# Kernel tuning notes

Measured on AMD Instinct MI355X. Metric: run time of the kernel, lower is better.

The kernel has to match this reference:

```python
import jax, jax.numpy as jnp
import numpy as np

MUL = 128   # multiplicity of every l in the input/output irreps
C   = 128   # channel count of the grid signal
LIN = 3     # lmax of irreps_in / irreps_out
LV  = 2     # VSH lmax = lmax - 1
NB  = 8     # res_beta  = 2*(lmax+1)
NA  = 7     # res_alpha = 2*lmax + 1
NLM = (LV + 1) ** 2  # 9 spherical-harmonic coefficients per component


def _sh_basis(L, Nb, Na):
    """Real orthonormal spherical harmonics on a Gauss-Legendre x uniform-alpha grid.
    Returns Y [(L+1)^2, Nb, Na] and quadrature weights qw [Nb, Na] so that
    sum_grid Y_i * Y_j * qw = delta_ij (exact at these resolutions)."""
    x, w = np.polynomial.legendre.leggauss(Nb)        # cos(beta) nodes/weights
    s = np.sqrt(1.0 - x * x)                          # sin(beta)
    alpha = 2.0 * np.pi * np.arange(Na) / Na
    # normalized associated Legendre Pbar[l, m, beta]
    P = np.zeros((L + 1, L + 1, Nb))
    P[0, 0] = np.sqrt(1.0 / (4.0 * np.pi))
    for m in range(1, L + 1):
        P[m, m] = -np.sqrt((2.0 * m + 1.0) / (2.0 * m)) * s * P[m - 1, m - 1]
    for m in range(0, L):
        P[m + 1, m] = np.sqrt(2.0 * m + 3.0) * x * P[m, m]
    for m in range(0, L + 1):
        for l in range(m + 2, L + 1):
            a = np.sqrt((4.0 * l * l - 1.0) / (l * l - m * m))
            b = np.sqrt(((l - 1.0) ** 2 - m * m) / (4.0 * (l - 1.0) ** 2 - 1.0))
            P[l, m] = a * (x * P[l - 1, m] - b * P[l - 2, m])
    Y = np.zeros(((L + 1) ** 2, Nb, Na))
    idx = 0
    for l in range(L + 1):
        for m in range(-l, l + 1):
            if m == 0:
                Y[idx] = P[l, 0][:, None] * np.ones(Na)[None, :]
            elif m > 0:
                Y[idx] = np.sqrt(2.0) * P[l, m][:, None] * np.cos(m * alpha)[None, :]
            else:
                Y[idx] = np.sqrt(2.0) * P[l, -m][:, None] * np.sin(-m * alpha)[None, :]
            idx += 1
    qw = (w[:, None] * (2.0 * np.pi / Na)) * np.ones(Na)[None, :]
    return Y.astype(np.float32), qw.astype(np.float32)


_Y_NP, _QW_NP = _sh_basis(LV, NB, NA)
_YJ = jnp.asarray(_Y_NP)              # [9, NB, NA]  synthesis basis
_YW = jnp.asarray(_Y_NP * _QW_NP)     # [9, NB, NA]  analysis (quadrature-weighted) basis


def _irreps_to_vsh_coeffs(x, W):
    """e3nn-style per-l Linear from input irreps (mul=MUL, l=0..LIN) to VSH coeffs.
    x: [B, MUL*sum(2l+1)], W: [LV+1, MUL, C, 4]. Input l-blocks above LV have no
    matching output irrep and are dropped (as e3nn Linear would).
    Returns [B, C, 4, NLM]."""
    coeffs, off = [], 0
    for l in range(LIN + 1):
        d = 2 * l + 1
        blk = x[:, off:off + MUL * d].reshape(-1, MUL, d)
        off += MUL * d
        if l <= LV:
            coeffs.append(jnp.einsum('bum,ucp->bcpm', blk, W[l]) / np.sqrt(MUL))
    return jnp.concatenate(coeffs, axis=-1)


def setup_inputs() -> dict:
    key = jax.random.key(0)
    k1, k2, k3, k4, k5 = jax.random.split(key, 5)
    B = 2048
    IN_DIM = MUL * sum(2 * l + 1 for l in range(LIN + 1))  # 2048
    return {
        'x1':   jax.random.normal(k1, (B, IN_DIM), dtype=jnp.float32),
        'x2':   jax.random.normal(k2, (B, IN_DIM), dtype=jnp.float32),
        'W1':   jax.random.normal(k3, (LV + 1, MUL, C, 4), dtype=jnp.float32),
        'W2':   jax.random.normal(k4, (LV + 1, MUL, C, 4), dtype=jnp.float32),
        'Wout': jax.random.normal(k5, (LV + 1, C, 4, MUL), dtype=jnp.float32),
    }


def reference(x1, x2, W1, W2, Wout):
    B = x1.shape[0]
    # equivariant linears -> VSH coefficients  [B, C, 4, 9]
    c1 = _irreps_to_vsh_coeffs(x1, W1)
    c2 = _irreps_to_vsh_coeffs(x2, W2)
    # to_vector_signal: SH synthesis per component -> [B, C, 4, NB, NA]
    s1 = jnp.einsum('bcpk,kxy->bcpxy', c1, _YJ)
    s2 = jnp.einsum('bcpk,kxy->bcpxy', c2, _YJ)
    # per-grid-point product: scalar mul on component 0, cross product on 1:4
    out_sig = jnp.concatenate(
        [s1[:, :, :1] * s2[:, :, :1],
         jnp.cross(s1[:, :, 1:], s2[:, :, 1:], axis=2)], axis=2)
    # from_vector_signal: quadrature SH analysis -> [B, C, 4, 9]
    c_out = jnp.einsum('bcpxy,kxy->bcpk', out_sig, _YW)
    # final equivariant linear back to output irreps (l<=LV paths; l=3 block has
    # no path from the VSH irreps so it is zero, matching e3nn Linear)
    blocks = []
    for l in range(LV + 1):
        d = 2 * l + 1
        cl = c_out[..., l * l:(l + 1) ** 2]                       # [B, C, 4, d]
        blk = jnp.einsum('bcpm,cpu->bum', cl, Wout[l]) / np.sqrt(4 * C)
        blocks.append(blk.reshape(B, MUL * d))
    blocks.append(jnp.zeros((B, MUL * (2 * LIN + 1)), dtype=x1.dtype))
    return jnp.concatenate(blocks, axis=-1)
```

## Files before the change

kernel.cpp:

```cpp
#include <hip/hip_runtime.h>
#include <math.h>

typedef short short8 __attribute__((ext_vector_type(8)));
typedef float f32x4 __attribute__((ext_vector_type(4)));

#define B_N 2048
#define NKM 9
#define CP 512
#define KU 128
#define INV_SQRT_MUL 0.08838834764831845f
#define INV_SQRT_4C  0.04419417382415922f

__device__ ushort g_xb1[NKM * B_N * KU];
__device__ ushort g_xb2[NKM * B_N * KU];
__device__ ushort g_W1bt[3 * CP * KU];
__device__ ushort g_W2bt[3 * CP * KU];
__device__ ushort g_Woutbt[3 * KU * CP];
__device__ ushort g_c1b[(size_t)B_N * NKM * CP];
__device__ ushort g_c2b[(size_t)B_N * NKM * CP];
__device__ ushort g_cb[(size_t)B_N * NKM * CP];

__device__ __forceinline__ ushort f2b(float f) {
    uint u = __float_as_uint(f);
    uint r = (u + 0x7fffu + ((u >> 16) & 1u)) >> 16;
    return (ushort)r;
}
__device__ __forceinline__ float b2f(uint h) {
    return __uint_as_float(h << 16);
}
__device__ __forceinline__ float pk_lo(uint u) { return __uint_as_float(u << 16); }
__device__ __forceinline__ float pk_hi(uint u) { return __uint_as_float(u & 0xffff0000u); }
__device__ __forceinline__ int l_of_km(int km) { return (km >= 4) ? 2 : (km >= 1 ? 1 : 0); }

__host__ __device__ constexpr int lof(int n) { return n >= 4 ? 2 : (n >= 1 ? 1 : 0); }
__host__ __device__ constexpr int mof(int n) { int l = lof(n); return n - l * l - l; }
__host__ __device__ constexpr bool gaunt_nz(int a, int b, int c) {
    int la = lof(a), lb = lof(b), lc = lof(c);
    if ((la + lb + lc) & 1) return false;
    if (lc > la + lb || la > lb + lc || lb > lc + la) return false;
    int ma = mof(a), mb = mof(b), mc = mof(c);
    int neg = (ma < 0) + (mb < 0) + (mc < 0);
    if (neg & 1) return false;
    int A = ma < 0 ? -ma : ma, Bm = mb < 0 ? -mb : mb, Cm = mc < 0 ? -mc : mc;
    return (A + Bm == Cm) || (Bm + Cm == A) || (Cm + A == Bm);
}
__host__ __device__ constexpr float gaunt_val(int a, int b, int c) {
    int x = a, y = b, z = c, t = 0;
    if (x > y) { t = x; x = y; y = t; }
    if (y > z) { t = y; y = z; z = t; }
    if (x > y) { t = x; x = y; y = t; }
    const float C00 = 0.28209479177387814f;
    const float A_  = 0.12615662610100802f;
    const float B_  = 0.25231325220201604f;
    const float C_  = 0.21850968611841584f;
    const float D_  = 0.18022375157286857f;
    const float E_  = 0.09011187578643429f;
    const float F_  = 0.15607834722743988f;
    if (x == 0) return C00;
    if (y <= 3) {
        if (z == 6) return (y == 2) ? B_ : -A_;
        if (z == 8) return (x == 1) ? -C_ : C_;
        return C_;
    }
    if (x == 4) return (y == 4) ? -D_ : F_;
    if (x == 5) return (z == 6) ? E_ : -F_;
    if (x == 6) return (y == 6) ? D_ : ((y == 7) ? E_ : -D_);
    return F_;
}
struct KEnt { int i, j; float v; };
struct KTab { KEnt e[16]; int n; };
__host__ __device__ constexpr KTab make_kt(int kk) {
    KTab t{};
    for (int i = 0; i < 9; ++i)
        for (int j = 0; j < 9; ++j)
            if (gaunt_nz(kk, i, j)) {
                t.e[t.n].i = i; t.e[t.n].j = j; t.e[t.n].v = gaunt_val(kk, i, j);
                ++t.n;
            }
    return t;
}

template <int KK>
__device__ __forceinline__ void gaunt_kk(const uint (&p1)[2][9], const uint (&p2)[2][9],
                                         ushort* __restrict__ w) {
    constexpr KTab T = make_kt(KK);
    float o0 = 0.f, o1 = 0.f, o2 = 0.f, o3 = 0.f;
    #pragma unroll
    for (int e = 0; e < T.n; ++e) {
        const int   i = T.e[e].i, j = T.e[e].j;
        const float g = T.e[e].v;
        float a0 = pk_lo(p1[0][i]), a1 = pk_hi(p1[0][i]);
        float a2 = pk_lo(p1[1][i]), a3 = pk_hi(p1[1][i]);
        float d0 = pk_lo(p2[0][j]), d1 = pk_hi(p2[0][j]);
        float d2 = pk_lo(p2[1][j]), d3 = pk_hi(p2[1][j]);
        o0 = fmaf(g, a0 * d0, o0);
        o1 = fmaf(g, fmaf(a2, d3, -(a3 * d2)), o1);
        o2 = fmaf(g, fmaf(a3, d1, -(a1 * d3)), o2);
        o3 = fmaf(g, fmaf(a1, d2, -(a2 * d1)), o3);
    }
    uint2 st;
    st.x = (uint)f2b(o0) | ((uint)f2b(o1) << 16);
    st.y = (uint)f2b(o2) | ((uint)f2b(o3) << 16);
    *(uint2*)&w[KK * CP] = st;
}

__global__ __launch_bounds__(256) void prep_kernel(const float* __restrict__ x1,
                                                   const float* __restrict__ x2,
                                                   const float* __restrict__ W1,
                                                   const float* __restrict__ W2,
                                                   const float* __restrict__ Wout,
                                                   float* __restrict__ out) {
    int bid = blockIdx.x, tid = threadIdx.x;
    if (bid >= B_N) {
        int idx = (bid - B_N) * 256 + tid;
        int l = idx >> 16;
        int r = idx & 65535;
        {
            int cp = r >> 7, u = r & 127;
            size_t src = (size_t)l * 65536 + (size_t)u * 512 + cp;
            g_W1bt[idx] = f2b(W1[src] * INV_SQRT_MUL);
            g_W2bt[idx] = f2b(W2[src] * INV_SQRT_MUL);
        }
        {
            int u = r >> 9, cp = r & 511;
            g_Woutbt[idx] = f2b(Wout[(size_t)l * 65536 + (size_t)cp * 128 + u] * INV_SQRT_4C);
        }
        return;
    }
    int b = bid;
    __shared__ float L1[2048], L2[2048];
    const float4* r1 = (const float4*)(x1 + (size_t)b * 2048);
    const float4* r2 = (const float4*)(x2 + (size_t)b * 2048);
    #pragma unroll
    for (int i = 0; i < 2; ++i) {
        int q = i * 256 + tid;
        *(float4*)&L1[q * 4] = r1[q];
        *(float4*)&L2[q * 4] = r2[q];
    }
    float4 z = make_float4(0.f, 0.f, 0.f, 0.f);
    if (tid < 224) *(float4*)&out[(size_t)b * 2048 + 1152 + tid * 4] = z;
    __syncthreads();
    #pragma unroll
    for (int i = 0; i < 9; ++i) {
        int e = i * 256 + tid;
        int field = e >= 1152;
        int r = e - field * 1152;
        int km = r >> 7, u = r & 127;
        int l = l_of_km(km);
        int col = l * l * 128 + u * (2 * l + 1) + (km - l * l);
        float v = field ? L2[col] : L1[col];
        ushort* dst = field ? g_xb2 : g_xb1;
        dst[(size_t)km * (B_N * KU) + (size_t)b * KU + u] = f2b(v);
    }
}

__global__ __launch_bounds__(256) void gemm_c_kernel() {
    __shared__ ushort As[64 * 128];
    __shared__ ushort Bs[128 * 128];
    int tid = threadIdx.x;
    int z = blockIdx.z;
    int field = (z >= NKM);
    int km = field ? z - NKM : z;
    int l = l_of_km(km);
    int n0 = blockIdx.x * 128, b0 = blockIdx.y * 64;
    const ushort* xa = (field ? g_xb2 : g_xb1) + (size_t)km * (B_N * KU);
    const ushort* wb = (field ? g_W2bt : g_W1bt) + (size_t)l * 65536;
    ushort* cdst = field ? g_c2b : g_c1b;

    #pragma unroll
    for (int it = 0; it < 4; ++it) {
        int i = it * 256 + tid;
        int row = i >> 4, kg = i & 15;
        int dst = row * 128 + ((kg ^ (row & 7)) << 3);
        *(short8*)&As[dst] = *(const short8*)&xa[(size_t)(b0 + row) * KU + (kg << 3)];
    }
    #pragma unroll
    for (int it = 0; it < 8; ++it) {
        int i = it * 256 + tid;
        int row = i >> 4, kg = i & 15;
        int dst = row * 128 + ((kg ^ (row & 7)) << 3);
        *(short8*)&Bs[dst] = *(const short8*)&wb[(size_t)(n0 + row) * KU + (kg << 3)];
    }
    __syncthreads();

    int lane = tid & 63, wid = tid >> 6, wr = wid >> 1, wc = wid & 1;
    f32x4 acc[2][4];
    #pragma unroll
    for (int i = 0; i < 2; ++i)
        #pragma unroll
        for (int j = 0; j < 4; ++j) acc[i][j] = (f32x4){0.f, 0.f, 0.f, 0.f};

    #pragma unroll
    for (int ks = 0; ks < 4; ++ks) {
        int kg = ks * 4 + (lane >> 4);
        short8 a[2], b[4];
        #pragma unroll
        for (int i = 0; i < 2; ++i) {
            int row = wr * 32 + i * 16 + (lane & 15);
            a[i] = *(const short8*)&As[row * 128 + ((kg ^ (row & 7)) << 3)];
        }
        #pragma unroll
        for (int j = 0; j < 4; ++j) {
            int row = wc * 64 + j * 16 + (lane & 15);
            b[j] = *(const short8*)&Bs[row * 128 + ((kg ^ (row & 7)) << 3)];
        }
        #pragma unroll
        for (int i = 0; i < 2; ++i)
            #pragma unroll
            for (int j = 0; j < 4; ++j)
                acc[i][j] = __builtin_amdgcn_mfma_f32_16x16x32_bf16(a[i], b[j], acc[i][j], 0, 0, 0);
    }

    #pragma unroll
    for (int i = 0; i < 2; ++i)
        #pragma unroll
        for (int j = 0; j < 4; ++j)
            #pragma unroll
            for (int r = 0; r < 4; ++r) {
                int row = b0 + wr * 32 + i * 16 + ((lane >> 4) << 2) + r;
                int col = n0 + wc * 64 + j * 16 + (lane & 15);
                cdst[((size_t)row * NKM + km) * CP + col] = f2b(acc[i][j][r]);
            }
}

__global__ __launch_bounds__(256) void middle_kernel() {
    int idx = blockIdx.x * 256 + threadIdx.x;
    int b = idx >> 7, c = idx & 127;
    const ushort* s1 = g_c1b + (size_t)b * (NKM * CP) + c * 4;
    const ushort* s2 = g_c2b + (size_t)b * (NKM * CP) + c * 4;

    uint p1[2][9], p2[2][9];
    #pragma unroll
    for (int k = 0; k < 9; ++k) {
        uint2 v1 = *(const uint2*)&s1[k * CP];
        uint2 v2 = *(const uint2*)&s2[k * CP];
        p1[0][k] = v1.x; p1[1][k] = v1.y;
        p2[0][k] = v2.x; p2[1][k] = v2.y;
    }

    ushort* w = g_cb + (size_t)b * (NKM * CP) + c * 4;
    gaunt_kk<0>(p1, p2, w);
    gaunt_kk<1>(p1, p2, w);
    gaunt_kk<2>(p1, p2, w);
    gaunt_kk<3>(p1, p2, w);
    gaunt_kk<4>(p1, p2, w);
    gaunt_kk<5>(p1, p2, w);
    gaunt_kk<6>(p1, p2, w);
    gaunt_kk<7>(p1, p2, w);
    gaunt_kk<8>(p1, p2, w);
}

__global__ __launch_bounds__(256) void out_gemm_kernel(float* __restrict__ out) {
    __shared__ ushort As[64 * 128];
    __shared__ ushort Bs[128 * 128];
    int tid = threadIdx.x;
    int km = blockIdx.y;
    int l = l_of_km(km);
    int mi = km - l * l, d = 2 * l + 1, OFF = 128 * l * l;
    int b0 = blockIdx.x * 64;

    int lane = tid & 63, wid = tid >> 6, wr = wid >> 1, wc = wid & 1;
    f32x4 acc[2][4];
    #pragma unroll
    for (int i = 0; i < 2; ++i)
        #pragma unroll
        for (int j = 0; j < 4; ++j) acc[i][j] = (f32x4){0.f, 0.f, 0.f, 0.f};

    for (int kc = 0; kc < 4; ++kc) {
        #pragma unroll
        for (int it = 0; it < 4; ++it) {
            int i = it * 256 + tid;
            int row = i >> 4, kg = i & 15;
            int dst = row * 128 + ((kg ^ (row & 7)) << 3);
            *(short8*)&As[dst] = *(const short8*)&g_cb[(size_t)(b0 + row) * (NKM * CP)
                                                       + (size_t)km * CP + kc * 128 + (kg << 3)];
        }
        #pragma unroll
        for (int it = 0; it < 8; ++it) {
            int i = it * 256 + tid;
            int row = i >> 4, kg = i & 15;
            int dst = row * 128 + ((kg ^ (row & 7)) << 3);
            *(short8*)&Bs[dst] = *(const short8*)&g_Woutbt[(size_t)l * 65536
                                                       + (size_t)row * CP + kc * 128 + (kg << 3)];
        }
        __syncthreads();
        #pragma unroll
        for (int ks = 0; ks < 4; ++ks) {
            int kg = ks * 4 + (lane >> 4);
            short8 a[2], b[4];
            #pragma unroll
            for (int i = 0; i < 2; ++i) {
                int row = wr * 32 + i * 16 + (lane & 15);
                a[i] = *(const short8*)&As[row * 128 + ((kg ^ (row & 7)) << 3)];
            }
            #pragma unroll
            for (int j = 0; j < 4; ++j) {
                int row = wc * 64 + j * 16 + (lane & 15);
                b[j] = *(const short8*)&Bs[row * 128 + ((kg ^ (row & 7)) << 3)];
            }
            #pragma unroll
            for (int i = 0; i < 2; ++i)
                #pragma unroll
                for (int j = 0; j < 4; ++j)
                    acc[i][j] = __builtin_amdgcn_mfma_f32_16x16x32_bf16(a[i], b[j], acc[i][j], 0, 0, 0);
        }
        __syncthreads();
    }

    #pragma unroll
    for (int i = 0; i < 2; ++i)
        #pragma unroll
        for (int j = 0; j < 4; ++j)
            #pragma unroll
            for (int r = 0; r < 4; ++r) {
                int row = b0 + wr * 32 + i * 16 + ((lane >> 4) << 2) + r;
                int u   = wc * 64 + j * 16 + (lane & 15);
                out[(size_t)row * 2048 + OFF + u * d + mi] = acc[i][j][r];
            }
}

extern "C" void kernel_launch(void* const* d_in, const int* in_sizes, int n_in,
                              void* d_out, int out_size, void* d_ws, size_t ws_size,
                              hipStream_t stream) {
    const float* x1   = (const float*)d_in[0];
    const float* x2   = (const float*)d_in[1];
    const float* W1   = (const float*)d_in[2];
    const float* W2   = (const float*)d_in[3];
    const float* Wout = (const float*)d_in[4];
    float* out = (float*)d_out;

    prep_kernel<<<B_N + 768, 256, 0, stream>>>(x1, x2, W1, W2, Wout, out);
    gemm_c_kernel<<<dim3(CP / 128, B_N / 64, 18), 256, 0, stream>>>();
    middle_kernel<<<(B_N * 128) / 256, 256, 0, stream>>>();
    out_gemm_kernel<<<dim3(B_N / 64, NKM), 256, 0, stream>>>(out);
}
```

Measured before the change: 57.34 us.

## Fuse coefficient GEMMs with Gaunt product kernel through shared memory staging

```diff
diff --git a/kernel.cpp b/kernel.cpp
--- a/kernel.cpp
+++ b/kernel.cpp
@@ -8,6 +8,7 @@
 #define NKM 9
 #define CP 512
 #define KU 128
+#define STG 132
 #define INV_SQRT_MUL 0.08838834764831845f
 #define INV_SQRT_4C  0.04419417382415922f
 
@@ -16,17 +17,12 @@
 __device__ ushort g_W1bt[3 * CP * KU];
 __device__ ushort g_W2bt[3 * CP * KU];
 __device__ ushort g_Woutbt[3 * KU * CP];
-__device__ ushort g_c1b[(size_t)B_N * NKM * CP];
-__device__ ushort g_c2b[(size_t)B_N * NKM * CP];
 __device__ ushort g_cb[(size_t)B_N * NKM * CP];
 
 __device__ __forceinline__ ushort f2b(float f) {
     uint u = __float_as_uint(f);
     uint r = (u + 0x7fffu + ((u >> 16) & 1u)) >> 16;
     return (ushort)r;
-}
-__device__ __forceinline__ float b2f(uint h) {
-    return __uint_as_float(h << 16);
 }
 __device__ __forceinline__ float pk_lo(uint u) { return __uint_as_float(u << 16); }
 __device__ __forceinline__ float pk_hi(uint u) { return __uint_as_float(u & 0xffff0000u); }
@@ -67,41 +63,43 @@
     if (x == 6) return (y == 6) ? D_ : ((y == 7) ? E_ : -D_);
     return F_;
 }
-struct KEnt { int i, j; float v; };
-struct KTab { KEnt e[16]; int n; };
-__host__ __device__ constexpr KTab make_kt(int kk) {
-    KTab t{};
-    for (int i = 0; i < 9; ++i)
+struct IEnt { int k, j; float v; };
+struct ITab { IEnt e[16]; int n; };
+__host__ __device__ constexpr ITab make_it(int ii) {
+    ITab t{};
+    for (int k = 0; k < 9; ++k)
         for (int j = 0; j < 9; ++j)
-            if (gaunt_nz(kk, i, j)) {
-                t.e[t.n].i = i; t.e[t.n].j = j; t.e[t.n].v = gaunt_val(kk, i, j);
+            if (gaunt_nz(k, ii, j)) {
+                t.e[t.n].k = k; t.e[t.n].j = j; t.e[t.n].v = gaunt_val(k, ii, j);
                 ++t.n;
             }
     return t;
 }
 
-template <int KK>
-__device__ __forceinline__ void gaunt_kk(const uint (&p1)[2][9], const uint (&p2)[2][9],
-                                         ushort* __restrict__ w) {
-    constexpr KTab T = make_kt(KK);
-    float o0 = 0.f, o1 = 0.f, o2 = 0.f, o3 = 0.f;
-    #pragma unroll
-    for (int e = 0; e < T.n; ++e) {
-        const int   i = T.e[e].i, j = T.e[e].j;
-        const float g = T.e[e].v;
-        float a0 = pk_lo(p1[0][i]), a1 = pk_hi(p1[0][i]);
-        float a2 = pk_lo(p1[1][i]), a3 = pk_hi(p1[1][i]);
-        float d0 = pk_lo(p2[0][j]), d1 = pk_hi(p2[0][j]);
-        float d2 = pk_lo(p2[1][j]), d3 = pk_hi(p2[1][j]);
-        o0 = fmaf(g, a0 * d0, o0);
-        o1 = fmaf(g, fmaf(a2, d3, -(a3 * d2)), o1);
-        o2 = fmaf(g, fmaf(a3, d1, -(a1 * d3)), o2);
-        o3 = fmaf(g, fmaf(a1, d2, -(a2 * d1)), o3);
-    }
-    uint2 st;
-    st.x = (uint)f2b(o0) | ((uint)f2b(o1) << 16);
-    st.y = (uint)f2b(o2) | ((uint)f2b(o3) << 16);
-    *(uint2*)&w[KK * CP] = st;
+template <int I>
+__device__ __forceinline__ void mid_step(const ushort* __restrict__ c1s,
+                                         int mb, int mc,
+                                         const float (&f2v)[2][9][4],
+                                         float (&o)[2][4][9]) {
+    constexpr ITab T = make_it(I);
+    #pragma unroll
+    for (int un = 0; un < 2; ++un) {
+        int cc = mc + un * 16;
+        uint2 v = *(const uint2*)&c1s[mb * STG + cc * 4];
+        float a0 = pk_lo(v.x), a1 = pk_hi(v.x);
+        float a2 = pk_lo(v.y), a3 = pk_hi(v.y);
+        #pragma unroll
+        for (int e = 0; e < T.n; ++e) {
+            const int   k = T.e[e].k, j = T.e[e].j;
+            const float g = T.e[e].v;
+            float d0 = f2v[un][j][0], d1 = f2v[un][j][1];
+            float d2 = f2v[un][j][2], d3 = f2v[un][j][3];
+            o[un][0][k] = fmaf(g, a0 * d0, o[un][0][k]);
+            o[un][1][k] = fmaf(g, fmaf(a2, d3, -(a3 * d2)), o[un][1][k]);
+            o[un][2][k] = fmaf(g, fmaf(a3, d1, -(a1 * d3)), o[un][2][k]);
+            o[un][3][k] = fmaf(g, fmaf(a1, d2, -(a2 * d1)), o[un][3][k]);
+        }
+    }
 }
 
 __global__ __launch_bounds__(256) void prep_kernel(const float* __restrict__ x1,
@@ -154,26 +152,14 @@
     }
 }
 
-__global__ __launch_bounds__(256) void gemm_c_kernel() {
-    __shared__ ushort As[64 * 128];
-    __shared__ ushort Bs[128 * 128];
-    int tid = threadIdx.x;
-    int z = blockIdx.z;
-    int field = (z >= NKM);
-    int km = field ? z - NKM : z;
-    int l = l_of_km(km);
-    int n0 = blockIdx.x * 128, b0 = blockIdx.y * 64;
-    const ushort* xa = (field ? g_xb2 : g_xb1) + (size_t)km * (B_N * KU);
-    const ushort* wb = (field ? g_W2bt : g_W1bt) + (size_t)l * 65536;
-    ushort* cdst = field ? g_c2b : g_c1b;
-
-    #pragma unroll
-    for (int it = 0; it < 4; ++it) {
-        int i = it * 256 + tid;
-        int row = i >> 4, kg = i & 15;
-        int dst = row * 128 + ((kg ^ (row & 7)) << 3);
-        *(short8*)&As[dst] = *(const short8*)&xa[(size_t)(b0 + row) * KU + (kg << 3)];
-    }
+__device__ __forceinline__ void load_A16(const ushort* __restrict__ xa, int b0,
+                                         int tid, ushort* As) {
+    int row = tid >> 4, kg = tid & 15;
+    int dst = row * 128 + ((kg ^ (row & 7)) << 3);
+    *(short8*)&As[dst] = *(const short8*)&xa[(size_t)(b0 + row) * KU + (kg << 3)];
+}
+__device__ __forceinline__ void load_B128(const ushort* __restrict__ wb, int n0,
+                                          int tid, ushort* Bs) {
     #pragma unroll
     for (int it = 0; it < 8; ++it) {
         int i = it * 256 + tid;
@@ -181,78 +167,108 @@
         int dst = row * 128 + ((kg ^ (row & 7)) << 3);
         *(short8*)&Bs[dst] = *(const short8*)&wb[(size_t)(n0 + row) * KU + (kg << 3)];
     }
-    __syncthreads();
-
-    int lane = tid & 63, wid = tid >> 6, wr = wid >> 1, wc = wid & 1;
-    f32x4 acc[2][4];
-    #pragma unroll
-    for (int i = 0; i < 2; ++i)
-        #pragma unroll
-        for (int j = 0; j < 4; ++j) acc[i][j] = (f32x4){0.f, 0.f, 0.f, 0.f};
-
+}
+__device__ __forceinline__ void gemm16x128(const ushort* As, const ushort* Bs,
+                                           int lane, int wid, ushort* stage) {
+    f32x4 acc0 = (f32x4){0.f, 0.f, 0.f, 0.f};
+    f32x4 acc1 = (f32x4){0.f, 0.f, 0.f, 0.f};
     #pragma unroll
     for (int ks = 0; ks < 4; ++ks) {
         int kg = ks * 4 + (lane >> 4);
-        short8 a[2], b[4];
-        #pragma unroll
-        for (int i = 0; i < 2; ++i) {
-            int row = wr * 32 + i * 16 + (lane & 15);
-            a[i] = *(const short8*)&As[row * 128 + ((kg ^ (row & 7)) << 3)];
-        }
-        #pragma unroll
-        for (int j = 0; j < 4; ++j) {
-            int row = wc * 64 + j * 16 + (lane & 15);
-            b[j] = *(const short8*)&Bs[row * 128 + ((kg ^ (row & 7)) << 3)];
-        }
-        #pragma unroll
-        for (int i = 0; i < 2; ++i)
-            #pragma unroll
-            for (int j = 0; j < 4; ++j)
-                acc[i][j] = __builtin_amdgcn_mfma_f32_16x16x32_bf16(a[i], b[j], acc[i][j], 0, 0, 0);
-    }
-
-    #pragma unroll
-    for (int i = 0; i < 2; ++i)
-        #pragma unroll
-        for (int j = 0; j < 4; ++j)
-            #pragma unroll
-            for (int r = 0; r < 4; ++r) {
-                int row = b0 + wr * 32 + i * 16 + ((lane >> 4) << 2) + r;
-                int col = n0 + wc * 64 + j * 16 + (lane & 15);
-                cdst[((size_t)row * NKM + km) * CP + col] = f2b(acc[i][j][r]);
-            }
-}
-
-__global__ __launch_bounds__(256) void middle_kernel() {
-    int idx = blockIdx.x * 256 + threadIdx.x;
-    int b = idx >> 7, c = idx & 127;
-    const ushort* s1 = g_c1b + (size_t)b * (NKM * CP) + c * 4;
-    const ushort* s2 = g_c2b + (size_t)b * (NKM * CP) + c * 4;
-
-    uint p1[2][9], p2[2][9];
+        int ar = lane & 15;
+        short8 a = *(const short8*)&As[ar * 128 + ((kg ^ (ar & 7)) << 3)];
+        int br0 = wid * 32 + (lane & 15);
+        short8 b0v = *(const short8*)&Bs[br0 * 128 + ((kg ^ (br0 & 7)) << 3)];
+        acc0 = __builtin_amdgcn_mfma_f32_16x16x32_bf16(a, b0v, acc0, 0, 0, 0);
+        int br1 = br0 + 16;
+        short8 b1v = *(const short8*)&Bs[br1 * 128 + ((kg ^ (br1 & 7)) << 3)];
+        acc1 = __builtin_amdgcn_mfma_f32_16x16x32_bf16(a, b1v, acc1, 0, 0, 0);
+    }
+    #pragma unroll
+    for (int r = 0; r < 4; ++r) {
+        int row = ((lane >> 4) << 2) + r;
+        stage[row * STG + wid * 32 + (lane & 15)]      = f2b(acc0[r]);
+        stage[row * STG + wid * 32 + 16 + (lane & 15)] = f2b(acc1[r]);
+    }
+}
+
+__global__ __launch_bounds__(256) void cmid_kernel() {
+    __shared__ ushort As[16 * 128];
+    __shared__ ushort Bs[128 * 128];
+    __shared__ ushort c1s[16 * STG];
+    __shared__ ushort c2s[9][16 * STG];
+
+    int tid = threadIdx.x;
+    int n0 = blockIdx.x * 128, b0 = blockIdx.y * 16;
+    int lane = tid & 63, wid = tid >> 6;
+    int mb = tid >> 4, mc = tid & 15;
+
+#define F2_STEP(KM) \
+    load_A16(g_xb2 + (size_t)(KM) * (B_N * KU), b0, tid, As); \
+    __syncthreads(); \
+    gemm16x128(As, Bs, lane, wid, &c2s[KM][0]); \
+    __syncthreads();
+
+    load_B128(g_W2bt + 0 * 65536, n0, tid, Bs);
+    F2_STEP(0)
+    load_B128(g_W2bt + 1 * 65536, n0, tid, Bs);
+    F2_STEP(1) F2_STEP(2) F2_STEP(3)
+    load_B128(g_W2bt + 2 * 65536, n0, tid, Bs);
+    F2_STEP(4) F2_STEP(5) F2_STEP(6) F2_STEP(7) F2_STEP(8)
+#undef F2_STEP
+
+    float f2v[2][9][4];
     #pragma unroll
     for (int k = 0; k < 9; ++k) {
-        uint2 v1 = *(const uint2*)&s1[k * CP];
-        uint2 v2 = *(const uint2*)&s2[k * CP];
-        p1[0][k] = v1.x; p1[1][k] = v1.y;
-        p2[0][k] = v2.x; p2[1][k] = v2.y;
-    }
-
-    ushort* w = g_cb + (size_t)b * (NKM * CP) + c * 4;
-    gaunt_kk<0>(p1, p2, w);
-    gaunt_kk<1>(p1, p2, w);
-    gaunt_kk<2>(p1, p2, w);
-    gaunt_kk<3>(p1, p2, w);
-    gaunt_kk<4>(p1, p2, w);
-    gaunt_kk<5>(p1, p2, w);
-    gaunt_kk<6>(p1, p2, w);
-    gaunt_kk<7>(p1, p2, w);
-    gaunt_kk<8>(p1, p2, w);
+        #pragma unroll
+        for (int un = 0; un < 2; ++un) {
+            int cc = mc + un * 16;
+            uint2 v = *(const uint2*)&c2s[k][mb * STG + cc * 4];
+            f2v[un][k][0] = pk_lo(v.x); f2v[un][k][1] = pk_hi(v.x);
+            f2v[un][k][2] = pk_lo(v.y); f2v[un][k][3] = pk_hi(v.y);
+        }
+    }
+
+    float o[2][4][9];
+    #pragma unroll
+    for (int un = 0; un < 2; ++un)
+        #pragma unroll
+        for (int p = 0; p < 4; ++p)
+            #pragma unroll
+            for (int k = 0; k < 9; ++k) o[un][p][k] = 0.f;
+
+#define F1_STEP(KM) \
+    load_A16(g_xb1 + (size_t)(KM) * (B_N * KU), b0, tid, As); \
+    __syncthreads(); \
+    gemm16x128(As, Bs, lane, wid, c1s); \
+    __syncthreads(); \
+    mid_step<KM>(c1s, mb, mc, f2v, o);
+
+    load_B128(g_W1bt + 0 * 65536, n0, tid, Bs);
+    F1_STEP(0)
+    load_B128(g_W1bt + 1 * 65536, n0, tid, Bs);
+    F1_STEP(1) F1_STEP(2) F1_STEP(3)
+    load_B128(g_W1bt + 2 * 65536, n0, tid, Bs);
+    F1_STEP(4) F1_STEP(5) F1_STEP(6) F1_STEP(7) F1_STEP(8)
+#undef F1_STEP
+
+    #pragma unroll
+    for (int un = 0; un < 2; ++un) {
+        int cc = mc + un * 16;
+        ushort* w = g_cb + (size_t)(b0 + mb) * (NKM * CP) + n0 + cc * 4;
+        #pragma unroll
+        for (int k = 0; k < 9; ++k) {
+            uint2 st;
+            st.x = (uint)f2b(o[un][0][k]) | ((uint)f2b(o[un][1][k]) << 16);
+            st.y = (uint)f2b(o[un][2][k]) | ((uint)f2b(o[un][3][k]) << 16);
+            *(uint2*)&w[(size_t)k * CP] = st;
+        }
+    }
 }
 
 __global__ __launch_bounds__(256) void out_gemm_kernel(float* __restrict__ out) {
-    __shared__ ushort As[64 * 128];
-    __shared__ ushort Bs[128 * 128];
+    __shared__ ushort Aso[64 * 128];
+    __shared__ ushort Bso[128 * 128];
     int tid = threadIdx.x;
     int km = blockIdx.y;
     int l = l_of_km(km);
@@ -272,7 +288,7 @@
             int i = it * 256 + tid;
             int row = i >> 4, kg = i & 15;
             int dst = row * 128 + ((kg ^ (row & 7)) << 3);
-            *(short8*)&As[dst] = *(const short8*)&g_cb[(size_t)(b0 + row) * (NKM * CP)
+            *(short8*)&Aso[dst] = *(const short8*)&g_cb[(size_t)(b0 + row) * (NKM * CP)
                                                        + (size_t)km * CP + kc * 128 + (kg << 3)];
         }
         #pragma unroll
@@ -280,7 +296,7 @@
             int i = it * 256 + tid;
             int row = i >> 4, kg = i & 15;
             int dst = row * 128 + ((kg ^ (row & 7)) << 3);
-            *(short8*)&Bs[dst] = *(const short8*)&g_Woutbt[(size_t)l * 65536
+            *(short8*)&Bso[dst] = *(const short8*)&g_Woutbt[(size_t)l * 65536
                                                        + (size_t)row * CP + kc * 128 + (kg << 3)];
         }
         __syncthreads();
@@ -291,12 +307,12 @@
             #pragma unroll
             for (int i = 0; i < 2; ++i) {
                 int row = wr * 32 + i * 16 + (lane & 15);
-                a[i] = *(const short8*)&As[row * 128 + ((kg ^ (row & 7)) << 3)];
+                a[i] = *(const short8*)&Aso[row * 128 + ((kg ^ (row & 7)) << 3)];
             }
             #pragma unroll
             for (int j = 0; j < 4; ++j) {
                 int row = wc * 64 + j * 16 + (lane & 15);
-                b[j] = *(const short8*)&Bs[row * 128 + ((kg ^ (row & 7)) << 3)];
+                b[j] = *(const short8*)&Bso[row * 128 + ((kg ^ (row & 7)) << 3)];
             }
             #pragma unroll
             for (int i = 0; i < 2; ++i)
@@ -330,7 +346,6 @@
     float* out = (float*)d_out;
 
     prep_kernel<<<B_N + 768, 256, 0, stream>>>(x1, x2, W1, W2, Wout, out);
-    gemm_c_kernel<<<dim3(CP / 128, B_N / 64, 18), 256, 0, stream>>>();
-    middle_kernel<<<(B_N * 128) / 256, 256, 0, stream>>>();
+    cmid_kernel<<<dim3(4, B_N / 16), 256, 0, stream>>>();
     out_gemm_kernel<<<dim3(B_N / 64, NKM), 256, 0, stream>>>(out);
 }
```

Result: slower. 64.84 us (+13.1%).
